# Kernel optimization log

Measured on AMD Instinct MI355X. Metric: run time of the kernel, lower is better.

Reference implementation:

```python
import jax, jax.numpy as jnp
import numpy as np

B = 8192      # batch
J = 32        # slots = 30 goal joints + traj + heading
C = 4         # target_cond_dim (3 input features + 1 validity flag)
D = 256       # splited_dim = latent_dim // J = 8192 // 32


def setup_inputs() -> dict:
    key = jax.random.key(0)
    k0, k1, k2, k3, k4, k5 = jax.random.split(key, 6)
    s1 = 1.0 / np.sqrt(C)  # torch Linear default init bound
    s2 = 1.0 / np.sqrt(D)
    return {
        "input": jax.random.normal(k0, (B, J, 3), jnp.float32),
        "validity": jax.random.randint(k1, (B, J), 0, 2, jnp.int32),
        # per-slot MLP params, stacked over the slot axis J
        "W1": jax.random.uniform(k2, (J, C, D), jnp.float32, -s1, s1),
        "b1": jax.random.uniform(k3, (J, D), jnp.float32, -s1, s1),
        "W2": jax.random.uniform(k4, (J, D, D), jnp.float32, -s2, s2),
        "b2": jax.random.uniform(k5, (J, D), jnp.float32, -s2, s2),
    }


def reference(input, validity, W1, b1, W2, b2):
    # mlp_input = cat([input, validity], -1) -> [B, J, 4]
    x = jnp.concatenate([input, validity[..., None].astype(input.dtype)], axis=-1)
    # per-slot Linear(4, D): batched over slots via einsum (replaces the Python loop)
    h = jnp.einsum('bjc,jcd->bjd', x, W1) + b1          # [B, J, D]
    h = jax.nn.silu(h)
    h = jnp.einsum('bjd,jde->bje', h, W2) + b2          # [B, J, D]
    # torch.cat(mlp_splits, dim=-1) == reshape since slots are contiguous
    return h.reshape(B, J * D)                           # [B, latent_dim]
```

## Files before the change

### kernel.cpp

```cpp
#include <hip/hip_runtime.h>

typedef short bf16x8 __attribute__((ext_vector_type(8)));
typedef float f32x4 __attribute__((ext_vector_type(4)));

#define AS1 __attribute__((address_space(1)))
#define AS3 __attribute__((address_space(3)))

__device__ __forceinline__ unsigned short f2bf(float f) {
  unsigned int u = __builtin_bit_cast(unsigned int, f);
  return (unsigned short)((u + 0x8000u) >> 16);
}

__global__ __launch_bounds__(256) void prep_w2t(const float* __restrict__ W2,
                                                unsigned char* __restrict__ w2t) {
  const int s = blockIdx.x;
  const int jc = blockIdx.y;
  const int j = jc >> 1, ch = jc & 1;
  const int t = threadIdx.x;
  __shared__ unsigned short lds[64 * 136];

  const float* src = W2 + (size_t)j * 65536 + (size_t)(s * 64) * 256 + ch * 128;
#pragma unroll
  for (int i = 0; i < 8; ++i) {
    const int idx4 = i * 256 + t;
    const int kk = idx4 >> 5;
    const int n4 = (idx4 & 31) << 2;
    const float4 v = *reinterpret_cast<const float4*>(src + kk * 256 + n4);
    unsigned short* p = &lds[kk * 136 + n4];
    p[0] = f2bf(v.x); p[1] = f2bf(v.y); p[2] = f2bf(v.z); p[3] = f2bf(v.w);
  }
  __syncthreads();

  unsigned char* dst = w2t + (((size_t)jc * 4 + s) << 14);
#pragma unroll
  for (int i = 0; i < 4; ++i) {
    const int slot = i * 256 + t;
    const int n = slot >> 3, u = slot & 7;
    const int kk0 = (u ^ (n & 7)) << 3;
    unsigned int w[4];
#pragma unroll
    for (int q = 0; q < 4; ++q) {
      const unsigned int lo = lds[(kk0 + 2 * q + 0) * 136 + n];
      const unsigned int hi = lds[(kk0 + 2 * q + 1) * 136 + n];
      w[q] = lo | (hi << 16);
    }
    *reinterpret_cast<uint4*>(dst + slot * 16) = make_uint4(w[0], w[1], w[2], w[3]);
  }
}

__global__ __launch_bounds__(512, 4) void fused_mlp(
    const float* __restrict__ input, const int* __restrict__ validity,
    const float* __restrict__ W1, const float* __restrict__ b1,
    const float* __restrict__ b2, const unsigned char* __restrict__ w2t,
    float* __restrict__ out) {
  __shared__ __align__(16) unsigned char smem[70656];
  const int bx = blockIdx.x;
  const int by = blockIdx.y;
  const int j = by >> 1, ch = by & 1;
  const int tid = threadIdx.x;
  const int wid = tid >> 6;
  const int lane = tid & 63;
  const int l15 = lane & 15, lg = lane >> 4;
  const int rowbase = (bx << 8) + (wid << 5);

  float xr[2][4];
#pragma unroll
  for (int mf = 0; mf < 2; ++mf) {
    const int row = rowbase + mf * 16 + l15;
    const float* ip = input + ((size_t)row * 32 + j) * 3;
    xr[mf][0] = ip[0]; xr[mf][1] = ip[1]; xr[mf][2] = ip[2];
    xr[mf][3] = (float)validity[row * 32 + j];
  }
  const float* b2j = b2 + (j << 8) + (ch << 7) + l15;
  float b2v[8];
#pragma unroll
  for (int nf = 0; nf < 8; ++nf) b2v[nf] = b2j[nf << 4];
  float4 wst = make_float4(0.f, 0.f, 0.f, 0.f);
  if (tid < 320) {
    const float* ws = (tid < 256) ? (W1 + (j << 10) + (tid << 2))
                                  : (b1 + (j << 8) + ((tid - 256) << 2));
    wst = *reinterpret_cast<const float4*>(ws);
  }

  const unsigned char* w2tj = w2t + ((size_t)by << 16);
#pragma unroll
  for (int it = 0; it < 8; ++it) {
    const int off = ((it << 3) + wid) << 10;
    __builtin_amdgcn_global_load_lds(
        (const AS1 unsigned int*)(w2tj + off + lane * 16),
        (AS3 unsigned int*)(smem + off), 16, 0, 0);
  }

  if (tid < 320) *reinterpret_cast<float4*>(smem + 65536 + (tid << 4)) = wst;

  f32x4 acc[2][8];
#pragma unroll
  for (int nf = 0; nf < 8; ++nf) {
    acc[0][nf] = f32x4{b2v[nf], b2v[nf], b2v[nf], b2v[nf]};
    acc[1][nf] = acc[0][nf];
  }

  asm volatile("s_waitcnt lgkmcnt(0)" ::: "memory");
  __builtin_amdgcn_s_barrier();

  const unsigned char* w1base = smem + 65536 + (lg << 5);
  const int q0 = (lg << 4) ^ ((l15 & 7) << 4);
  const unsigned char* rA = smem + l15 * 128 + q0;
  const unsigned char* rB = smem + l15 * 128 + (q0 ^ 64);

  const size_t colbase = (size_t)(j << 8) + (ch << 7) + l15;

#pragma unroll
  for (int s = 0; s < 4; ++s) {
    bf16x8 af[2][2];
#pragma unroll
    for (int kf2 = 0; kf2 < 2; ++kf2) {
      const int kf = 2 * s + kf2;
#pragma unroll
      for (int half = 0; half < 2; ++half) {
        const int im = kf * 128 + half * 16;
        const f32x4 w0 = *reinterpret_cast<const f32x4*>(w1base + im);
        const f32x4 w1v = *reinterpret_cast<const f32x4*>(w1base + 1024 + im);
        const f32x4 w2v = *reinterpret_cast<const f32x4*>(w1base + 2048 + im);
        const f32x4 w3v = *reinterpret_cast<const f32x4*>(w1base + 3072 + im);
        const f32x4 bb = *reinterpret_cast<const f32x4*>(w1base + 4096 + im);
#pragma unroll
        for (int mf = 0; mf < 2; ++mf) {
#pragma unroll
          for (int i = 0; i < 4; ++i) {
            float z = bb[i];
            z = fmaf(xr[mf][0], w0[i], z);
            z = fmaf(xr[mf][1], w1v[i], z);
            z = fmaf(xr[mf][2], w2v[i], z);
            z = fmaf(xr[mf][3], w3v[i], z);
            const float h = z * __builtin_amdgcn_rcpf(1.0f + __expf(-z));
            af[kf2][mf][half * 4 + i] = (short)f2bf(h);
          }
        }
      }
    }

    if (s == 0)      asm volatile("s_waitcnt vmcnt(6)" ::: "memory");
    else if (s == 1) asm volatile("s_waitcnt vmcnt(4)" ::: "memory");
    else if (s == 2) asm volatile("s_waitcnt vmcnt(2)" ::: "memory");
    else             asm volatile("s_waitcnt vmcnt(0)" ::: "memory");
    __builtin_amdgcn_s_barrier();

    const int base = s << 14;
#pragma unroll
    for (int nf = 0; nf < 8; ++nf) {
      const bf16x8 bf0 = *reinterpret_cast<const bf16x8*>(rA + base + nf * 2048);
      const bf16x8 bf1 = *reinterpret_cast<const bf16x8*>(rB + base + nf * 2048);
      acc[0][nf] = __builtin_amdgcn_mfma_f32_16x16x32_bf16(af[0][0], bf0, acc[0][nf], 0, 0, 0);
      acc[1][nf] = __builtin_amdgcn_mfma_f32_16x16x32_bf16(af[0][1], bf0, acc[1][nf], 0, 0, 0);
      acc[0][nf] = __builtin_amdgcn_mfma_f32_16x16x32_bf16(af[1][0], bf1, acc[0][nf], 0, 0, 0);
      acc[1][nf] = __builtin_amdgcn_mfma_f32_16x16x32_bf16(af[1][1], bf1, acc[1][nf], 0, 0, 0);
    }
  }

#pragma unroll
  for (int mf = 0; mf < 2; ++mf) {
#pragma unroll
    for (int r = 0; r < 4; ++r) {
      const int row = rowbase + mf * 16 + (lg << 2) + r;
      float* pr = out + (size_t)row * 8192 + colbase;
#pragma unroll
      for (int nf = 0; nf < 8; ++nf) pr[nf << 4] = acc[mf][nf][r];
    }
  }
}

extern "C" void kernel_launch(void* const* d_in, const int* in_sizes, int n_in,
                              void* d_out, int out_size, void* d_ws, size_t ws_size,
                              hipStream_t stream) {
  (void)in_sizes; (void)n_in; (void)out_size; (void)ws_size;
  const float* input    = (const float*)d_in[0];
  const int*   validity = (const int*)d_in[1];
  const float* W1       = (const float*)d_in[2];
  const float* b1       = (const float*)d_in[3];
  const float* W2       = (const float*)d_in[4];
  const float* b2       = (const float*)d_in[5];
  float* out = (float*)d_out;
  unsigned char* w2t = (unsigned char*)d_ws;

  prep_w2t<<<dim3(4, 64), 256, 0, stream>>>(W2, w2t);
  fused_mlp<<<dim3(32, 64), 512, 0, stream>>>(input, validity, W1, b1, b2, w2t, out);
}
```

Before: 89.46 us.

## Switch to fp16 MFMA with packed half2 SiLU and interleaved compute

Converts W2 and the hidden activations from bf16 to fp16 and computes the first layer plus SiLU with packed half2 FMAs, exp2 and rcp. This roughly halves the VALU cost of the on-the-fly activation generation. The activation for each k-fragment is now produced just before its MFMAs and the MFMA regions run under raised s_setprio, so VALU and matrix work can interleave. The grid is flattened with the slot index varying fastest, and b2 is staged through LDS. Computing the first layer in fp16 reduces precision and risks overflow for large pre-activations.

```diff
diff --git a/kernel.cpp b/kernel.cpp
--- a/kernel.cpp
+++ b/kernel.cpp
@@ -1,14 +1,15 @@
 #include <hip/hip_runtime.h>
-
-typedef short bf16x8 __attribute__((ext_vector_type(8)));
+#include <hip/hip_fp16.h>
+
+typedef _Float16 f16x8 __attribute__((ext_vector_type(8)));
 typedef float f32x4 __attribute__((ext_vector_type(4)));
 
 #define AS1 __attribute__((address_space(1)))
 #define AS3 __attribute__((address_space(3)))
 
-__device__ __forceinline__ unsigned short f2bf(float f) {
-  unsigned int u = __builtin_bit_cast(unsigned int, f);
-  return (unsigned short)((u + 0x8000u) >> 16);
+__device__ __forceinline__ unsigned short f2h(float f) {
+  _Float16 h = (_Float16)f;
+  return __builtin_bit_cast(unsigned short, h);
 }
 
 __global__ __launch_bounds__(256) void prep_w2t(const float* __restrict__ W2,
@@ -27,7 +28,7 @@
     const int n4 = (idx4 & 31) << 2;
     const float4 v = *reinterpret_cast<const float4*>(src + kk * 256 + n4);
     unsigned short* p = &lds[kk * 136 + n4];
-    p[0] = f2bf(v.x); p[1] = f2bf(v.y); p[2] = f2bf(v.z); p[3] = f2bf(v.w);
+    p[0] = f2h(v.x); p[1] = f2h(v.y); p[2] = f2h(v.z); p[3] = f2h(v.w);
   }
   __syncthreads();
 
@@ -48,14 +49,46 @@
   }
 }
 
+__device__ __forceinline__ void jit_af(const unsigned char* w1base,
+                                       const __half2 xh[2][4], int kf,
+                                       f16x8 af[2]) {
+  const int o = kf << 6;
+  const uint4 w0 = *reinterpret_cast<const uint4*>(w1base + o);
+  const uint4 w1v = *reinterpret_cast<const uint4*>(w1base + 512 + o);
+  const uint4 w2v = *reinterpret_cast<const uint4*>(w1base + 1024 + o);
+  const uint4 w3v = *reinterpret_cast<const uint4*>(w1base + 1536 + o);
+  const uint4 bb = *reinterpret_cast<const uint4*>(w1base + 2048 + o);
+  const __half2 one2 = __float2half2_rn(1.0f);
+  const __half2 nl2e = __float2half2_rn(-1.44269504f);
+#pragma unroll
+  for (int mf = 0; mf < 2; ++mf) {
+    unsigned int hw[4];
+#pragma unroll
+    for (int p = 0; p < 4; ++p) {
+      __half2 z = __builtin_bit_cast(__half2, (&bb.x)[p]);
+      z = __hfma2(xh[mf][0], __builtin_bit_cast(__half2, (&w0.x)[p]), z);
+      z = __hfma2(xh[mf][1], __builtin_bit_cast(__half2, (&w1v.x)[p]), z);
+      z = __hfma2(xh[mf][2], __builtin_bit_cast(__half2, (&w2v.x)[p]), z);
+      z = __hfma2(xh[mf][3], __builtin_bit_cast(__half2, (&w3v.x)[p]), z);
+      const __half2 e = h2exp2(__hmul2(z, nl2e));
+      const __half2 sig = h2rcp(__hadd2(one2, e));
+      const __half2 h = __hmul2(z, sig);
+      hw[p] = __builtin_bit_cast(unsigned int, h);
+    }
+    const uint4 u4 = make_uint4(hw[0], hw[1], hw[2], hw[3]);
+    af[mf] = __builtin_bit_cast(f16x8, u4);
+  }
+}
+
 __global__ __launch_bounds__(512, 4) void fused_mlp(
     const float* __restrict__ input, const int* __restrict__ validity,
     const float* __restrict__ W1, const float* __restrict__ b1,
     const float* __restrict__ b2, const unsigned char* __restrict__ w2t,
     float* __restrict__ out) {
-  __shared__ __align__(16) unsigned char smem[70656];
-  const int bx = blockIdx.x;
-  const int by = blockIdx.y;
+  __shared__ __align__(16) unsigned char smem[68608];
+  const int bid = blockIdx.x;
+  const int by = bid & 63;
+  const int bx = bid >> 6;
   const int j = by >> 1, ch = by & 1;
   const int tid = threadIdx.x;
   const int wid = tid >> 6;
@@ -71,15 +104,18 @@
     xr[mf][0] = ip[0]; xr[mf][1] = ip[1]; xr[mf][2] = ip[2];
     xr[mf][3] = (float)validity[row * 32 + j];
   }
-  const float* b2j = b2 + (j << 8) + (ch << 7) + l15;
-  float b2v[8];
-#pragma unroll
-  for (int nf = 0; nf < 8; ++nf) b2v[nf] = b2j[nf << 4];
-  float4 wst = make_float4(0.f, 0.f, 0.f, 0.f);
-  if (tid < 320) {
-    const float* ws = (tid < 256) ? (W1 + (j << 10) + (tid << 2))
-                                  : (b1 + (j << 8) + ((tid - 256) << 2));
-    wst = *reinterpret_cast<const float4*>(ws);
+  float4 wa = make_float4(0.f, 0.f, 0.f, 0.f);
+  float4 wb = make_float4(0.f, 0.f, 0.f, 0.f);
+  if (tid < 128) {
+    const float* ws = W1 + (j << 10) + (tid << 3);
+    wa = *reinterpret_cast<const float4*>(ws);
+    wb = *reinterpret_cast<const float4*>(ws + 4);
+  } else if (tid < 160) {
+    const float* ws = b1 + (j << 8) + ((tid - 128) << 3);
+    wa = *reinterpret_cast<const float4*>(ws);
+    wb = *reinterpret_cast<const float4*>(ws + 4);
+  } else if (tid < 192) {
+    wa = *reinterpret_cast<const float4*>(b2 + (j << 8) + (ch << 7) + ((tid - 160) << 2));
   }
 
   const unsigned char* w2tj = w2t + ((size_t)by << 16);
@@ -91,54 +127,46 @@
         (AS3 unsigned int*)(smem + off), 16, 0, 0);
   }
 
-  if (tid < 320) *reinterpret_cast<float4*>(smem + 65536 + (tid << 4)) = wst;
-
-  f32x4 acc[2][8];
-#pragma unroll
-  for (int nf = 0; nf < 8; ++nf) {
-    acc[0][nf] = f32x4{b2v[nf], b2v[nf], b2v[nf], b2v[nf]};
-    acc[1][nf] = acc[0][nf];
-  }
+  if (tid < 160) {
+    f16x8 hv;
+    hv[0] = (_Float16)wa.x; hv[1] = (_Float16)wa.y;
+    hv[2] = (_Float16)wa.z; hv[3] = (_Float16)wa.w;
+    hv[4] = (_Float16)wb.x; hv[5] = (_Float16)wb.y;
+    hv[6] = (_Float16)wb.z; hv[7] = (_Float16)wb.w;
+    *reinterpret_cast<f16x8*>(smem + 65536 + (tid << 4)) = hv;
+  } else if (tid < 192) {
+    *reinterpret_cast<float4*>(smem + 65536 + 2560 + ((tid - 160) << 4)) = wa;
+  }
+
+  __half2 xh[2][4];
+#pragma unroll
+  for (int mf = 0; mf < 2; ++mf)
+#pragma unroll
+    for (int c = 0; c < 4; ++c) xh[mf][c] = __float2half2_rn(xr[mf][c]);
 
   asm volatile("s_waitcnt lgkmcnt(0)" ::: "memory");
   __builtin_amdgcn_s_barrier();
 
-  const unsigned char* w1base = smem + 65536 + (lg << 5);
+  const unsigned char* w1base = smem + 65536 + (lg << 4);
+  const unsigned char* b2base = smem + 65536 + 2560 + (l15 << 2);
   const int q0 = (lg << 4) ^ ((l15 & 7) << 4);
   const unsigned char* rA = smem + l15 * 128 + q0;
   const unsigned char* rB = smem + l15 * 128 + (q0 ^ 64);
 
+  f32x4 acc[2][8];
+#pragma unroll
+  for (int nf = 0; nf < 8; ++nf) {
+    const float b = *reinterpret_cast<const float*>(b2base + (nf << 6));
+    acc[0][nf] = f32x4{b, b, b, b};
+    acc[1][nf] = acc[0][nf];
+  }
+
   const size_t colbase = (size_t)(j << 8) + (ch << 7) + l15;
+  f16x8 af[2];
 
 #pragma unroll
   for (int s = 0; s < 4; ++s) {
-    bf16x8 af[2][2];
-#pragma unroll
-    for (int kf2 = 0; kf2 < 2; ++kf2) {
-      const int kf = 2 * s + kf2;
-#pragma unroll
-      for (int half = 0; half < 2; ++half) {
-        const int im = kf * 128 + half * 16;
-        const f32x4 w0 = *reinterpret_cast<const f32x4*>(w1base + im);
-        const f32x4 w1v = *reinterpret_cast<const f32x4*>(w1base + 1024 + im);
-        const f32x4 w2v = *reinterpret_cast<const f32x4*>(w1base + 2048 + im);
-        const f32x4 w3v = *reinterpret_cast<const f32x4*>(w1base + 3072 + im);
-        const f32x4 bb = *reinterpret_cast<const f32x4*>(w1base + 4096 + im);
-#pragma unroll
-        for (int mf = 0; mf < 2; ++mf) {
-#pragma unroll
-          for (int i = 0; i < 4; ++i) {
-            float z = bb[i];
-            z = fmaf(xr[mf][0], w0[i], z);
-            z = fmaf(xr[mf][1], w1v[i], z);
-            z = fmaf(xr[mf][2], w2v[i], z);
-            z = fmaf(xr[mf][3], w3v[i], z);
-            const float h = z * __builtin_amdgcn_rcpf(1.0f + __expf(-z));
-            af[kf2][mf][half * 4 + i] = (short)f2bf(h);
-          }
-        }
-      }
-    }
+    jit_af(w1base, xh, 2 * s, af);
 
     if (s == 0)      asm volatile("s_waitcnt vmcnt(6)" ::: "memory");
     else if (s == 1) asm volatile("s_waitcnt vmcnt(4)" ::: "memory");
@@ -147,15 +175,24 @@
     __builtin_amdgcn_s_barrier();
 
     const int base = s << 14;
+    __builtin_amdgcn_s_setprio(1);
 #pragma unroll
     for (int nf = 0; nf < 8; ++nf) {
-      const bf16x8 bf0 = *reinterpret_cast<const bf16x8*>(rA + base + nf * 2048);
-      const bf16x8 bf1 = *reinterpret_cast<const bf16x8*>(rB + base + nf * 2048);
-      acc[0][nf] = __builtin_amdgcn_mfma_f32_16x16x32_bf16(af[0][0], bf0, acc[0][nf], 0, 0, 0);
-      acc[1][nf] = __builtin_amdgcn_mfma_f32_16x16x32_bf16(af[0][1], bf0, acc[1][nf], 0, 0, 0);
-      acc[0][nf] = __builtin_amdgcn_mfma_f32_16x16x32_bf16(af[1][0], bf1, acc[0][nf], 0, 0, 0);
-      acc[1][nf] = __builtin_amdgcn_mfma_f32_16x16x32_bf16(af[1][1], bf1, acc[1][nf], 0, 0, 0);
-    }
+      const f16x8 bf0 = *reinterpret_cast<const f16x8*>(rA + base + nf * 2048);
+      acc[0][nf] = __builtin_amdgcn_mfma_f32_16x16x32_f16(af[0], bf0, acc[0][nf], 0, 0, 0);
+      acc[1][nf] = __builtin_amdgcn_mfma_f32_16x16x32_f16(af[1], bf0, acc[1][nf], 0, 0, 0);
+    }
+    __builtin_amdgcn_s_setprio(0);
+
+    jit_af(w1base, xh, 2 * s + 1, af);
+    __builtin_amdgcn_s_setprio(1);
+#pragma unroll
+    for (int nf = 0; nf < 8; ++nf) {
+      const f16x8 bf1 = *reinterpret_cast<const f16x8*>(rB + base + nf * 2048);
+      acc[0][nf] = __builtin_amdgcn_mfma_f32_16x16x32_f16(af[0], bf1, acc[0][nf], 0, 0, 0);
+      acc[1][nf] = __builtin_amdgcn_mfma_f32_16x16x32_f16(af[1], bf1, acc[1][nf], 0, 0, 0);
+    }
+    __builtin_amdgcn_s_setprio(0);
   }
 
 #pragma unroll
@@ -184,5 +221,5 @@
   unsigned char* w2t = (unsigned char*)d_ws;
 
   prep_w2t<<<dim3(4, 64), 256, 0, stream>>>(W2, w2t);
-  fused_mlp<<<dim3(32, 64), 512, 0, stream>>>(input, validity, W1, b1, b2, w2t, out);
-}
+  fused_mlp<<<2048, 512, 0, stream>>>(input, validity, W1, b1, b2, w2t, out);
+}
```

Result: faster. 79.61 us, median of 2 (-11.0%).
